# Performance work log

Hardware: AMD Instinct MI355X
Metric: run time of the kernel (lower is better)

The kernel has to match this reference:

```python
import jax, jax.numpy as jnp
import numpy as np

THRES = 0.5
EPS = 1e-8
FACTOR = 5


def _row_normalize(mx):
    # torch: rowsum over last dim, 1/rowsum with inf->0, diag @ mx == row scaling
    r_inv = 1.0 / mx.sum(-1)
    r_inv = jnp.where(jnp.isinf(r_inv), 0.0, r_inv)
    return mx * r_inv[..., None]


def _build_adj(feat):
    # cosine-similarity adjacency over rows of feat [B,N,D] -> [B,N,N]
    fn = feat / jnp.maximum(jnp.linalg.norm(feat, axis=-1, keepdims=True), EPS)
    sim = jnp.einsum('bnd,bmd->bnm', fn, fn)
    adj = (sim > THRES).astype(feat.dtype)
    adjT = jnp.swapaxes(adj, 1, 2)
    m = (adjT > adj).astype(feat.dtype)
    adj = adj + adjT * m - adj * m  # symmetric OR
    return _row_normalize(adj + jnp.eye(adj.shape[1], dtype=feat.dtype))


def _gcn(x, adj, w1, b1, w2, b2):
    # standard 2-layer pygcn: out = adj @ (x @ W) + b, relu between, dropout=0
    h = jax.nn.relu(jnp.einsum('bnm,bmf->bnf', adj, x @ w1) + b1)
    return jnp.einsum('bnm,bmf->bnf', adj, h @ w2) + b2


def setup_inputs() -> dict:
    key = jax.random.key(0)
    ks = jax.random.split(key, 13)
    B, C, HT = 1024, 64, 128   # batch, in_dim channels, height == feature_len
    FL, NH = 128, 8            # GCN nfeat/nclass, nhid
    s = lambda i, shape: jax.random.normal(ks[i], shape, jnp.float32) * 0.1
    return dict(
        x=jax.random.normal(ks[0], (B, C, HT), jnp.float32),
        wq=s(1, (C, C)), bq=s(2, (C,)),
        wk=s(3, (C, C)), bk=s(4, (C,)),
        wv=s(5, (C, C)), bv=s(6, (C,)),
        gw1=s(7, (FL, NH)), gb1=s(8, (NH,)),
        gw2=s(9, (NH, FL)), gb2=s(10, (FL,)),
        gamma=jax.random.normal(ks[11], (), jnp.float32),
        index_sample=jax.random.randint(ks[12], (HT, 25), 0, HT),  # (L_Q_inner, sample_k)
    )


def reference(x, wq, bq, wk, bk, wv, bv, gw1, gb1, gw2, gb2, gamma, index_sample):
    # 1x1 Conv1d projections: [B,C,H] -> [B,C,H]
    q = jnp.einsum('oc,bch->boh', wq, x) + bq[None, :, None]
    k = jnp.einsum('oc,bch->boh', wk, x) + bk[None, :, None]
    v = jnp.einsum('oc,bch->boh', wv, x) + bv[None, :, None]

    def branch(f):
        # source uses self.gcn_query for all three branches (faithful)
        return _gcn(_row_normalize(f), _build_adj(f), gw1, gb1, gw2, gb2)

    queries, keys, values = branch(q), branch(k), branch(v)
    B, L_Q, H = queries.shape        # [B, 64, 128]
    u = min(FACTOR * int(np.ceil(np.log(L_Q))), L_Q)  # n_top = 25

    # ProbSparse _prob_QK: inner view (B, Hn=64, Lk=128)
    Lk = keys.shape[2]
    Kg = keys[:, :, index_sample]                        # [B,64,Lk,S] gather
    qk_sample = jnp.einsum('bhl,bhls->bhs', queries, Kg)  # [B,64,S]
    M = qk_sample.max(-1) - qk_sample.sum(-1) / Lk        # [B,64]
    _, m_top = jax.lax.top_k(M, u)                        # [B,u] indices over node dim
    q_red = jnp.take_along_axis(queries, m_top[:, :, None], axis=1)  # [B,u,128]
    scores = jnp.einsum('bud,bnd->bun', q_red, keys) * (1.0 / np.sqrt(H))

    # mask_flag=True -> initial context is cumsum over nodes
    context = jnp.cumsum(values, axis=-2)                 # [B,64,128]
    attn = jax.nn.softmax(scores, axis=-1)
    upd = jnp.einsum('bun,bnd->bud', attn, values)        # [B,u,128]
    context = context.at[jnp.arange(B)[:, None], m_top].set(upd)
    return gamma * context + x
```

## Files before the change

kernel.cpp:

```cpp
#include <hip/hip_runtime.h>
#include <math.h>

#define T 1024
#define FS 132
#define FSQ 33
#define AS 68

typedef __attribute__((ext_vector_type(8)))  short short8;
typedef __attribute__((ext_vector_type(4)))  float f32x4;
typedef __attribute__((ext_vector_type(16))) float f32x16;
typedef __attribute__((ext_vector_type(4)))  unsigned u32x4;
typedef __attribute__((ext_vector_type(2)))  unsigned u32x2;

__device__ __forceinline__ void fma4(float4& a, float s, const float4 b) {
  a.x = fmaf(s, b.x, a.x);
  a.y = fmaf(s, b.y, a.y);
  a.z = fmaf(s, b.z, a.z);
  a.w = fmaf(s, b.w, a.w);
}
__device__ __forceinline__ unsigned bf16rne(float f) {
  unsigned u = __float_as_uint(f);
  return (u + 0x7FFFu + ((u >> 16) & 1u)) >> 16;
}
__device__ __forceinline__ void split3(float4 a, float4 b, short8& vh, short8& vm, short8& vl) {
  const float xs[8] = {a.x, a.y, a.z, a.w, b.x, b.y, b.z, b.w};
#pragma unroll
  for (int e = 0; e < 8; ++e) {
    float x = xs[e];
    unsigned h = bf16rne(x);
    float r1 = x - __uint_as_float(h << 16);
    unsigned m = bf16rne(r1);
    float r2 = r1 - __uint_as_float(m << 16);
    unsigned l2 = bf16rne(r2);
    vh[e] = (short)h; vm[e] = (short)m; vl[e] = (short)l2;
  }
}
__device__ __forceinline__ void split2(float4 a, float4 b, short8& vh, short8& vl) {
  const float xs[8] = {a.x, a.y, a.z, a.w, b.x, b.y, b.z, b.w};
#pragma unroll
  for (int e = 0; e < 8; ++e) {
    float x = xs[e];
    unsigned h = bf16rne(x);
    float r1 = x - __uint_as_float(h << 16);
    unsigned l2 = bf16rne(r1);
    vh[e] = (short)h; vl[e] = (short)l2;
  }
}
__device__ __forceinline__ f32x16 mm32(short8 a, short8 b, f32x16 c) {
  return __builtin_amdgcn_mfma_f32_32x32x16_bf16(a, b, c, 0, 0, 0);
}
__device__ __forceinline__ f32x4 mm16(short8 a, short8 b, f32x4 c) {
  return __builtin_amdgcn_mfma_f32_16x16x32_bf16(a, b, c, 0, 0, 0);
}

__global__ __launch_bounds__(T) void gcn_ssa_kernel(
    const float* __restrict__ x,
    const float* __restrict__ wq, const float* __restrict__ bq,
    const float* __restrict__ wk, const float* __restrict__ bk,
    const float* __restrict__ wv, const float* __restrict__ bv,
    const float* __restrict__ gw1, const float* __restrict__ gb1,
    const float* __restrict__ gw2, const float* __restrict__ gb2,
    const float* __restrict__ gammap, const int* __restrict__ idxg,
    float* __restrict__ out)
{
  const int b = blockIdx.x, tid = threadIdx.x;
  const int l = tid & 63;
  const int wid = tid >> 6;
  const float* xb = x + (size_t)b * 8192;
  float* outb = out + (size_t)b * 8192;

  __shared__ __align__(16) float fq[64 * FS];
  __shared__ __align__(16) float fk[64 * FS];
  __shared__ __align__(16) float fv[64 * FS];
  __shared__ __align__(16) float U[11904];
  __shared__ __align__(16) float gw1T[16 * FS];
  __shared__ __align__(16) float gb1s[8];
  __shared__ __align__(16) float gb2s[128];
  __shared__ float rinv_s[3][64], nrm_s[3][64], rinv2_s[3][64];
  __shared__ int mte[32];

  float4* fq4 = (float4*)fq;
  float4* fk4 = (float4*)fk;
  float4* fv4 = (float4*)fv;

  {
    const float4* xg = (const float4*)xb;
    for (int i = tid; i < 2048; i += T) {
      int c = i & 63, hq = i >> 6;
      float4 v = xg[c * 32 + hq];
      int h = hq * 4;
      U[(h + 0) * AS + c] = v.x;
      U[(h + 1) * AS + c] = v.y;
      U[(h + 2) * AS + c] = v.z;
      U[(h + 3) * AS + c] = v.w;
    }
    if (tid < 192) U[8704 + tid] = (tid < 64) ? bq[tid] : (tid < 128) ? bk[tid - 64] : bv[tid - 128];
    for (int i = tid; i < 2048; i += T) {
      int j = i >> 7, h = i & 127;
      gw1T[j * FS + h] = (j < 8) ? gw1[h * 8 + j] : 0.f;
    }
    if (tid < 8) gb1s[tid] = gb1[tid];
    if (tid < 128) gb2s[tid] = gb2[tid];
  }
  __syncthreads();

  if (wid < 12) {
    const int p = wid >> 2, strip = wid & 3;
    const float* wsel = (p == 0) ? wq : (p == 1) ? wk : wv;
    float* fdst = (p == 0) ? fq : (p == 1) ? fk : fv;
    const int lr = l & 31, kg = (l >> 5) * 4;
    const int h = strip * 32 + lr;
    f32x16 acc0 = (f32x16)0.f, acc1 = (f32x16)0.f;
    for (int ks = 0; ks < 4; ++ks) {
      int kb = ks * 16;
      float4 b0 = *(const float4*)(U + h * AS + kb + kg);
      float4 b1 = *(const float4*)(U + h * AS + kb + 8 + kg);
      short8 bh, bm, bl;
      split3(b0, b1, bh, bm, bl);
      float4 a0 = *(const float4*)(wsel + lr * 64 + kb + kg);
      float4 a1 = *(const float4*)(wsel + lr * 64 + kb + 8 + kg);
      short8 ah, am, al;
      split3(a0, a1, ah, am, al);
      acc0 = mm32(ah, bh, acc0); acc0 = mm32(ah, bm, acc0); acc0 = mm32(am, bh, acc0);
      acc0 = mm32(ah, bl, acc0); acc0 = mm32(al, bh, acc0); acc0 = mm32(am, bm, acc0);
      a0 = *(const float4*)(wsel + (32 + lr) * 64 + kb + kg);
      a1 = *(const float4*)(wsel + (32 + lr) * 64 + kb + 8 + kg);
      split3(a0, a1, ah, am, al);
      acc1 = mm32(ah, bh, acc1); acc1 = mm32(ah, bm, acc1); acc1 = mm32(am, bh, acc1);
      acc1 = mm32(ah, bl, acc1); acc1 = mm32(al, bh, acc1); acc1 = mm32(am, bm, acc1);
    }
#pragma unroll
    for (int reg = 0; reg < 16; ++reg) {
      int ro = (reg & 3) + 8 * (reg >> 2) + 4 * (l >> 5);
      fdst[ro * FS + h] = acc0[reg] + U[8704 + p * 64 + ro];
      fdst[(32 + ro) * FS + h] = acc1[reg] + U[8704 + p * 64 + 32 + ro];
    }
  }
  __syncthreads();

  {
    int row = tid >> 4, g = tid & 15;
#pragma unroll
    for (int br = 0; br < 3; ++br) {
      const float4* f4b = (br == 0) ? fq4 : (br == 1) ? fk4 : fv4;
      float4 aa = f4b[row * FSQ + 2 * g];
      float4 cc = f4b[row * FSQ + 2 * g + 1];
      float s0 = aa.x + aa.y + aa.z + aa.w + cc.x + cc.y + cc.z + cc.w;
      float s1 = aa.x * aa.x + aa.y * aa.y + aa.z * aa.z + aa.w * aa.w +
                 cc.x * cc.x + cc.y * cc.y + cc.z * cc.z + cc.w * cc.w;
      for (int off = 8; off; off >>= 1) {
        s0 += __shfl_xor(s0, off);
        s1 += __shfl_xor(s1, off);
      }
      if (g == 0) {
        rinv_s[br][row] = (s0 == 0.0f) ? 0.0f : (1.0f / s0);
        nrm_s[br][row] = 1.0f / fmaxf(sqrtf(s1), 1e-8f);
      }
    }
  }
  __syncthreads();

  unsigned short* adjw = (unsigned short*)U;
  float* t1T = U + 6912;
  float* hT  = U + 8544;
  float* gsm = U + 10176;

  if (wid < 12) {
    int br = wid >> 2, tile = wid & 3;
    const float* f = (br == 0) ? fq : (br == 1) ? fk : fv;
    int r0 = (tile >> 1) * 32, c0 = (tile & 1) * 32;
    int lr = l & 31, kg = (l >> 5) * 4;
    f32x16 acc = (f32x16)0.f;
    for (int ks = 0; ks < 8; ++ks) {
      int kb = ks * 16;
      float4 a0 = *(const float4*)(f + (r0 + lr) * FS + kb + kg);
      float4 a1 = *(const float4*)(f + (r0 + lr) * FS + kb + 8 + kg);
      float4 b0 = *(const float4*)(f + (c0 + lr) * FS + kb + kg);
      float4 b1 = *(const float4*)(f + (c0 + lr) * FS + kb + 8 + kg);
      short8 ah, am, al, bh, bm, bl;
      split3(a0, a1, ah, am, al);
      split3(b0, b1, bh, bm, bl);
      acc = mm32(ah, bh, acc); acc = mm32(ah, bm, acc); acc = mm32(am, bh, acc);
      acc = mm32(ah, bl, acc); acc = mm32(al, bh, acc); acc = mm32(am, bm, acc);
    }
    float nm = nrm_s[br][c0 + lr];
#pragma unroll
    for (int reg = 0; reg < 16; ++reg) {
      int rowg = r0 + (reg & 3) + 8 * (reg >> 2) + 4 * (l >> 5);
      int m = c0 + lr;
      float sim = acc[reg] * nrm_s[br][rowg] * nm;
      unsigned short e = (sim > 0.5f) ? (unsigned short)0x3F80 : (unsigned short)0;
      if (rowg == m) e = (sim > 0.5f) ? (unsigned short)0x4000 : (unsigned short)0x3F80;
      adjw[(br * 64 + rowg) * 72 + m] = e;
    }
  } else {
    int u = wid - 12;
    int j15 = l & 15, kg4 = (l >> 4) * 4;
    short8 gbh[4], gbm[4], gbl[4];
#pragma unroll
    for (int ks = 0; ks < 4; ++ks) {
      int kb = ks * 32;
      float4 b0 = *(const float4*)(gw1T + j15 * FS + kb + kg4);
      float4 b1 = *(const float4*)(gw1T + j15 * FS + kb + 16 + kg4);
      split3(b0, b1, gbh[ks], gbm[ks], gbl[ks]);
    }
#pragma unroll
    for (int i = 0; i < 3; ++i) {
      int tl = u * 3 + i;
      int br = tl >> 2, mt = tl & 3;
      const float* f = (br == 0) ? fq : (br == 1) ? fk : fv;
      f32x4 acc = (f32x4)0.f;
      for (int ks = 0; ks < 4; ++ks) {
        int kb = ks * 32;
        float4 a0 = *(const float4*)(f + (mt * 16 + j15) * FS + kb + kg4);
        float4 a1 = *(const float4*)(f + (mt * 16 + j15) * FS + kb + 16 + kg4);
        short8 ah, am, al;
        split3(a0, a1, ah, am, al);
        acc = mm16(ah, gbh[ks], acc); acc = mm16(ah, gbm[ks], acc); acc = mm16(am, gbh[ks], acc);
        acc = mm16(ah, gbl[ks], acc); acc = mm16(al, gbh[ks], acc); acc = mm16(am, gbm[ks], acc);
      }
      if (j15 < 8) {
#pragma unroll
        for (int r = 0; r < 4; ++r) {
          int n = mt * 16 + (l >> 4) * 4 + r;
          t1T[(br * 8 + j15) * AS + n] = acc[r] * rinv_s[br][n];
        }
      }
    }
  }
  __syncthreads();

  if (tid < 768) {
    int rid = tid >> 2, g = tid & 3;
    int br = rid >> 6, n = rid & 63;
    const unsigned short* rp = adjw + (br * 64 + n) * 72 + g * 16;
    u32x4 v0 = *(const u32x4*)rp;
    u32x4 v1 = *(const u32x4*)(rp + 8);
    unsigned wds[8] = {v0.x, v0.y, v0.z, v0.w, v1.x, v1.y, v1.z, v1.w};
    float s = 0.f;
#pragma unroll
    for (int e = 0; e < 8; ++e) {
      s += __uint_as_float(wds[e] << 16);
      s += __uint_as_float(wds[e] & 0xFFFF0000u);
    }
    s += __shfl_xor(s, 1);
    s += __shfl_xor(s, 2);
    if (g == 0) rinv2_s[br][n] = 1.0f / s;
  }
  __syncthreads();

  if (tid < 768) {
    int br = wid >> 2, mt = wid & 3;
    int j15 = l & 15, kg4 = (l >> 4) * 4;
    int arow = br * 64 + mt * 16 + j15;
    f32x4 acc = (f32x4)0.f;
#pragma unroll
    for (int ks = 0; ks < 2; ++ks) {
      int kb = ks * 32;
      u32x2 lo = *(const u32x2*)(adjw + arow * 72 + kb + kg4);
      u32x2 hi = *(const u32x2*)(adjw + arow * 72 + kb + 16 + kg4);
      u32x4 cc; cc.x = lo.x; cc.y = lo.y; cc.z = hi.x; cc.w = hi.y;
      short8 af = __builtin_bit_cast(short8, cc);
      float4 b0 = *(const float4*)(t1T + (br * 8 + j15) * AS + kb + kg4);
      float4 b1 = *(const float4*)(t1T + (br * 8 + j15) * AS + kb + 16 + kg4);
      short8 bh, bm, bl;
      split3(b0, b1, bh, bm, bl);
      acc = mm16(af, bh, acc); acc = mm16(af, bm, acc); acc = mm16(af, bl, acc);
    }
    if (j15 < 8) {
      float g1 = gb1s[j15];
#pragma unroll
      for (int r = 0; r < 4; ++r) {
        int n = mt * 16 + (l >> 4) * 4 + r;
        hT[(br * 8 + j15) * AS + n] = fmaxf(fmaf(acc[r], rinv2_s[br][n], g1), 0.0f);
      }
    }
  }
  __syncthreads();

  if (tid < 768) {
    int br = wid >> 2, mt = wid & 3;
    int j15 = l & 15, kg4 = (l >> 4) * 4;
    int arow = br * 64 + mt * 16 + j15;
    f32x4 acc = (f32x4)0.f;
#pragma unroll
    for (int ks = 0; ks < 2; ++ks) {
      int kb = ks * 32;
      u32x2 lo = *(const u32x2*)(adjw + arow * 72 + kb + kg4);
      u32x2 hi = *(const u32x2*)(adjw + arow * 72 + kb + 16 + kg4);
      u32x4 cc; cc.x = lo.x; cc.y = lo.y; cc.z = hi.x; cc.w = hi.y;
      short8 af = __builtin_bit_cast(short8, cc);
      float4 b0 = *(const float4*)(hT + (br * 8 + j15) * AS + kb + kg4);
      float4 b1 = *(const float4*)(hT + (br * 8 + j15) * AS + kb + 16 + kg4);
      short8 bh, bm, bl;
      split3(b0, b1, bh, bm, bl);
      acc = mm16(af, bh, acc); acc = mm16(af, bm, acc); acc = mm16(af, bl, acc);
    }
    if (j15 < 8) {
#pragma unroll
      for (int r = 0; r < 4; ++r) {
        int n = mt * 16 + (l >> 4) * 4 + r;
        gsm[(br * 64 + n) * 8 + j15] = acc[r] * rinv2_s[br][n];
      }
    }
  }
  __syncthreads();

  {
    int n0 = tid >> 5, hq = tid & 31;
    float4 wreg[8];
#pragma unroll
    for (int j = 0; j < 8; ++j) wreg[j] = ((const float4*)gw2)[j * 32 + hq];
    float4 bquad = ((const float4*)gb2s)[hq];
#pragma unroll
    for (int br = 0; br < 3; ++br) {
      float4* f4b = (br == 0) ? fq4 : (br == 1) ? fk4 : fv4;
#pragma unroll
      for (int half = 0; half < 2; ++half) {
        int n = n0 + 32 * half;
        const float* g = gsm + (br * 64 + n) * 8;
        float4 g0 = *(const float4*)g;
        float4 g1 = *(const float4*)(g + 4);
        float4 a = bquad;
        fma4(a, g0.x, wreg[0]); fma4(a, g0.y, wreg[1]); fma4(a, g0.z, wreg[2]); fma4(a, g0.w, wreg[3]);
        fma4(a, g1.x, wreg[4]); fma4(a, g1.y, wreg[5]); fma4(a, g1.z, wreg[6]); fma4(a, g1.w, wreg[7]);
        f4b[n * FSQ + hq] = a;
      }
    }
  }
  __syncthreads();

  float* kT = U;
  float* Pp = U + 8704;
  {
    const int c = tid >> 6;
    const int n = tid & 63;
    float4 v0 = fk4[n * FSQ + 2 * c];
    float4 v1 = fk4[n * FSQ + 2 * c + 1];
    const float* p0 = (const float*)&v0;
    const float* p1 = (const float*)&v1;
#pragma unroll
    for (int e = 0; e < 4; ++e) kT[(8 * c + e) * AS + n] = p0[e];
#pragma unroll
    for (int e = 0; e < 4; ++e) kT[(8 * c + 4 + e) * AS + n] = p1[e];
  }
  __syncthreads();

  const float gamma = *gammap;
  if (tid < 128) {
    const int w = tid >> 6, n = l;
    float acc[25];
#pragma unroll
    for (int s = 0; s < 25; ++s) acc[s] = 0.f;
    const float* qrow = fq + n * FS + w * 64;
    for (int lb = 0; lb < 16; ++lb) {
      float4 qv = *(const float4*)(qrow + 4 * lb);
      const float* qp = (const float*)&qv;
#pragma unroll
      for (int i = 0; i < 4; ++i) {
        const float qs = qp[i];
        const int base = __builtin_amdgcn_readfirstlane((w * 64 + 4 * lb + i) * 25);
#pragma unroll
        for (int s = 0; s < 25; ++s) {
          acc[s] = fmaf(qs, kT[idxg[base + s] * AS + n], acc[s]);
        }
      }
    }
    float* P = Pp + w * 1600;
#pragma unroll
    for (int s = 0; s < 25; ++s) P[s * 64 + n] = acc[s];
  } else if (tid < 256) {
    const int h = tid - 128;
    float acc = 0.f;
    for (int n = 0; n < 64; ++n) {
      acc += fv[n * FS + h];
      outb[n * 128 + h] = fmaf(gamma, acc, xb[n * 128 + h]);
    }
  }
  __syncthreads();

  if (tid < 64) {
    if (tid >= 25 && tid < 32) mte[tid] = 0;
    const float* P0 = Pp;
    const float* P1 = Pp + 1600;
    float mx = -INFINITY, su = 0.f;
#pragma unroll
    for (int s = 0; s < 25; ++s) {
      float vsum = P0[s * 64 + tid] + P1[s * 64 + tid];
      mx = fmaxf(mx, vsum);
      su += vsum;
    }
    float v = mx - su * (1.0f / 128.0f);
    for (int it = 0; it < 25; ++it) {
      float bv2 = v;
      int bi = tid;
#pragma unroll
      for (int off = 32; off > 0; off >>= 1) {
        float ov = __shfl_xor(bv2, off);
        int oi = __shfl_xor(bi, off);
        if (ov > bv2 || (ov == bv2 && oi < bi)) { bv2 = ov; bi = oi; }
      }
      if (tid == 0) mte[it] = bi;
      if (tid == bi) v = -INFINITY;
    }
  }
  __syncthreads();

  float* sc = U + 8704;
  float* vT = U;
  if (tid < 128) {
    const int wsc = tid >> 6;
    const int lr = l & 31;
    const int kg = (l >> 5) * 4;
    const int qr = mte[lr];
    const float scale = 0.08838834764831845f;
    f32x16 acc = (f32x16)0.f;
    for (int ks = 0; ks < 8; ++ks) {
      int kb = ks * 16;
      float4 a0 = *(const float4*)(fq + qr * FS + kb + kg);
      float4 a1 = *(const float4*)(fq + qr * FS + kb + 8 + kg);
      float4 b0 = *(const float4*)(fk + (wsc * 32 + lr) * FS + kb + kg);
      float4 b1 = *(const float4*)(fk + (wsc * 32 + lr) * FS + kb + 8 + kg);
      short8 ah, al2, bh, bl;
      split2(a0, a1, ah, al2);
      split2(b0, b1, bh, bl);
      acc = mm32(ah, bh, acc);
      acc = mm32(ah, bl, acc);
      acc = mm32(al2, bh, acc);
    }
#pragma unroll
    for (int reg = 0; reg < 16; ++reg) {
      int uu = (reg & 3) + 8 * (reg >> 2) + 4 * (l >> 5);
      if (uu < 25) sc[uu * AS + wsc * 32 + lr] = acc[reg] * scale;
    }
  } else {
    for (int i = tid - 128; i < 8192; i += 896) {
      int h2 = i >> 6, n = i & 63;
      vT[h2 * AS + n] = fv[n * FS + h2];
    }
  }
  __syncthreads();

  if (tid < 400) {
    int u = tid >> 4, g = tid & 15;
    float4* s4 = (float4*)(sc + u * AS);
    float4 v = s4[g];
    float mx = fmaxf(fmaxf(v.x, v.y), fmaxf(v.z, v.w));
    for (int off = 8; off; off >>= 1) mx = fmaxf(mx, __shfl_xor(mx, off));
    float4 e;
    e.x = __expf(v.x - mx); e.y = __expf(v.y - mx);
    e.z = __expf(v.z - mx); e.w = __expf(v.w - mx);
    float su = e.x + e.y + e.z + e.w;
    for (int off = 8; off; off >>= 1) su += __shfl_xor(su, off);
    float inv = 1.0f / su;
    e.x *= inv; e.y *= inv; e.z *= inv; e.w *= inv;
    s4[g] = e;
  }
  __syncthreads();

  if (tid < 512) {
    const int w8 = tid >> 6;
    const int li = l & 15;
    const int kg4 = (l >> 4) * 4;
#pragma unroll
    for (int i = 0; i < 2; ++i) {
      int t = w8 * 2 + i;
      int ut = t >> 3, ht = t & 7;
      int u = ut * 16 + li;
      f32x4 acc = (f32x4)0.f;
#pragma unroll
      for (int ks = 0; ks < 2; ++ks) {
        int kb = ks * 32;
        float4 a0 = *(const float4*)(sc + u * AS + kb + kg4);
        float4 a1 = *(const float4*)(sc + u * AS + kb + 16 + kg4);
        float4 b0 = *(const float4*)(vT + (ht * 16 + li) * AS + kb + kg4);
        float4 b1 = *(const float4*)(vT + (ht * 16 + li) * AS + kb + 16 + kg4);
        short8 ah, al2, bh, bl;
        split2(a0, a1, ah, al2);
        split2(b0, b1, bh, bl);
        acc = mm16(ah, bh, acc);
        acc = mm16(ah, bl, acc);
        acc = mm16(al2, bh, acc);
      }
      int hcol = ht * 16 + li;
#pragma unroll
      for (int r = 0; r < 4; ++r) {
        int uu = ut * 16 + (l >> 4) * 4 + r;
        if (uu < 25) {
          int row = mte[uu];
          int o = row * 128 + hcol;
          outb[o] = fmaf(gamma, acc[r], xb[o]);
        }
      }
    }
  }
}

extern "C" void kernel_launch(void* const* d_in, const int* in_sizes, int n_in,
                              void* d_out, int out_size, void* d_ws, size_t ws_size,
                              hipStream_t stream) {
  const float* x   = (const float*)d_in[0];
  const float* wq  = (const float*)d_in[1];
  const float* bq  = (const float*)d_in[2];
  const float* wk  = (const float*)d_in[3];
  const float* bk  = (const float*)d_in[4];
  const float* wv  = (const float*)d_in[5];
  const float* bv  = (const float*)d_in[6];
  const float* gw1 = (const float*)d_in[7];
  const float* gb1 = (const float*)d_in[8];
  const float* gw2 = (const float*)d_in[9];
  const float* gb2 = (const float*)d_in[10];
  const float* gm  = (const float*)d_in[11];
  const int* idx   = (const int*)d_in[12];
  float* out = (float*)d_out;
  int B = in_sizes[0] / (64 * 128);
  hipLaunchKernelGGL(gcn_ssa_kernel, dim3(B), dim3(T), 0, stream,
                     x, wq, bq, wk, bk, wv, bv, gw1, gb1, gw2, gb2, gm, idx, out);
}
```

Baseline: 296.6 us.

## Exploit adjacency symmetry, fuse rowsum into GCN stage, restage ProbSparse sampling

The similarity matmul now computes only the two diagonal 32x32 tiles and one off-diagonal tile per branch, mirroring the result into the transposed position, since the matrix is symmetric. That frees warps, which take on the X@W1 tiles. The adjacency row-sum is folded into the first GCN aggregation stage, removing one barrier. The sample indices are staged into LDS as packed ushorts, the Q-K sampling loop is reorganised so each lane handles two rows and half the samples, and the V transpose moves earlier to overlap with top-k selection. These changes cut redundant MFMA work, a synchronisation and repeated global index loads, at the cost of more complex indexing and possible LDS bank conflicts on the mirrored stores.

```diff
diff --git a/kernel.cpp b/kernel.cpp
--- a/kernel.cpp
+++ b/kernel.cpp
@@ -165,37 +165,58 @@
   float* hT  = U + 8544;
   float* gsm = U + 10176;
 
-  if (wid < 12) {
-    int br = wid >> 2, tile = wid & 3;
+  if (wid < 9) {
+    const int br = wid / 3, t3 = wid % 3;
     const float* f = (br == 0) ? fq : (br == 1) ? fk : fv;
-    int r0 = (tile >> 1) * 32, c0 = (tile & 1) * 32;
-    int lr = l & 31, kg = (l >> 5) * 4;
+    const int lr = l & 31, kg = (l >> 5) * 4;
     f32x16 acc = (f32x16)0.f;
-    for (int ks = 0; ks < 8; ++ks) {
-      int kb = ks * 16;
-      float4 a0 = *(const float4*)(f + (r0 + lr) * FS + kb + kg);
-      float4 a1 = *(const float4*)(f + (r0 + lr) * FS + kb + 8 + kg);
-      float4 b0 = *(const float4*)(f + (c0 + lr) * FS + kb + kg);
-      float4 b1 = *(const float4*)(f + (c0 + lr) * FS + kb + 8 + kg);
-      short8 ah, am, al, bh, bm, bl;
-      split3(a0, a1, ah, am, al);
-      split3(b0, b1, bh, bm, bl);
-      acc = mm32(ah, bh, acc); acc = mm32(ah, bm, acc); acc = mm32(am, bh, acc);
-      acc = mm32(ah, bl, acc); acc = mm32(al, bh, acc); acc = mm32(am, bm, acc);
-    }
-    float nm = nrm_s[br][c0 + lr];
-#pragma unroll
-    for (int reg = 0; reg < 16; ++reg) {
-      int rowg = r0 + (reg & 3) + 8 * (reg >> 2) + 4 * (l >> 5);
-      int m = c0 + lr;
-      float sim = acc[reg] * nrm_s[br][rowg] * nm;
-      unsigned short e = (sim > 0.5f) ? (unsigned short)0x3F80 : (unsigned short)0;
-      if (rowg == m) e = (sim > 0.5f) ? (unsigned short)0x4000 : (unsigned short)0x3F80;
-      adjw[(br * 64 + rowg) * 72 + m] = e;
+    if (t3 < 2) {
+      const int r0 = t3 * 32;
+      for (int ks = 0; ks < 8; ++ks) {
+        int kb = ks * 16;
+        float4 a0 = *(const float4*)(f + (r0 + lr) * FS + kb + kg);
+        float4 a1 = *(const float4*)(f + (r0 + lr) * FS + kb + 8 + kg);
+        short8 h, m, lo;
+        split3(a0, a1, h, m, lo);
+        acc = mm32(h, h, acc); acc = mm32(h, m, acc); acc = mm32(m, h, acc);
+        acc = mm32(h, lo, acc); acc = mm32(lo, h, acc); acc = mm32(m, m, acc);
+      }
+      float nm = nrm_s[br][r0 + lr];
+#pragma unroll
+      for (int reg = 0; reg < 16; ++reg) {
+        int rowg = r0 + (reg & 3) + 8 * (reg >> 2) + 4 * (l >> 5);
+        int m = r0 + lr;
+        float sim = acc[reg] * nrm_s[br][rowg] * nm;
+        unsigned short e = (sim > 0.5f) ? (unsigned short)0x3F80 : (unsigned short)0;
+        if (rowg == m) e = (sim > 0.5f) ? (unsigned short)0x4000 : (unsigned short)0x3F80;
+        adjw[(br * 64 + rowg) * 72 + m] = e;
+      }
+    } else {
+      for (int ks = 0; ks < 8; ++ks) {
+        int kb = ks * 16;
+        float4 a0 = *(const float4*)(f + lr * FS + kb + kg);
+        float4 a1 = *(const float4*)(f + lr * FS + kb + 8 + kg);
+        float4 b0 = *(const float4*)(f + (32 + lr) * FS + kb + kg);
+        float4 b1 = *(const float4*)(f + (32 + lr) * FS + kb + 8 + kg);
+        short8 ah, am, al, bh, bm, bl;
+        split3(a0, a1, ah, am, al);
+        split3(b0, b1, bh, bm, bl);
+        acc = mm32(ah, bh, acc); acc = mm32(ah, bm, acc); acc = mm32(am, bh, acc);
+        acc = mm32(ah, bl, acc); acc = mm32(al, bh, acc); acc = mm32(am, bm, acc);
+      }
+      float nm = nrm_s[br][32 + lr];
+#pragma unroll
+      for (int reg = 0; reg < 16; ++reg) {
+        int rowg = (reg & 3) + 8 * (reg >> 2) + 4 * (l >> 5);
+        int m = 32 + lr;
+        float sim = acc[reg] * nrm_s[br][rowg] * nm;
+        unsigned short e = (sim > 0.5f) ? (unsigned short)0x3F80 : (unsigned short)0;
+        adjw[(br * 64 + rowg) * 72 + m] = e;
+        adjw[(br * 64 + m) * 72 + rowg] = e;
+      }
     }
   } else {
-    int u = wid - 12;
-    int j15 = l & 15, kg4 = (l >> 4) * 4;
+    const int j15 = l & 15, kg4 = (l >> 4) * 4;
     short8 gbh[4], gbm[4], gbl[4];
 #pragma unroll
     for (int ks = 0; ks < 4; ++ks) {
@@ -205,54 +226,58 @@
       split3(b0, b1, gbh[ks], gbm[ks], gbl[ks]);
     }
 #pragma unroll
-    for (int i = 0; i < 3; ++i) {
-      int tl = u * 3 + i;
-      int br = tl >> 2, mt = tl & 3;
-      const float* f = (br == 0) ? fq : (br == 1) ? fk : fv;
-      f32x4 acc = (f32x4)0.f;
-      for (int ks = 0; ks < 4; ++ks) {
-        int kb = ks * 32;
-        float4 a0 = *(const float4*)(f + (mt * 16 + j15) * FS + kb + kg4);
-        float4 a1 = *(const float4*)(f + (mt * 16 + j15) * FS + kb + 16 + kg4);
-        short8 ah, am, al;
-        split3(a0, a1, ah, am, al);
-        acc = mm16(ah, gbh[ks], acc); acc = mm16(ah, gbm[ks], acc); acc = mm16(am, gbh[ks], acc);
-        acc = mm16(ah, gbl[ks], acc); acc = mm16(al, gbh[ks], acc); acc = mm16(am, gbm[ks], acc);
-      }
-      if (j15 < 8) {
-#pragma unroll
-        for (int r = 0; r < 4; ++r) {
-          int n = mt * 16 + (l >> 4) * 4 + r;
-          t1T[(br * 8 + j15) * AS + n] = acc[r] * rinv_s[br][n];
+    for (int rep = 0; rep < 2; ++rep) {
+      int t = (wid - 9) + rep * 7;
+      if (t < 12) {
+        int br = t >> 2, mt = t & 3;
+        const float* f = (br == 0) ? fq : (br == 1) ? fk : fv;
+        f32x4 acc = (f32x4)0.f;
+        for (int ks = 0; ks < 4; ++ks) {
+          int kb = ks * 32;
+          float4 a0 = *(const float4*)(f + (mt * 16 + j15) * FS + kb + kg4);
+          float4 a1 = *(const float4*)(f + (mt * 16 + j15) * FS + kb + 16 + kg4);
+          short8 ah, am, al;
+          split3(a0, a1, ah, am, al);
+          acc = mm16(ah, gbh[ks], acc); acc = mm16(ah, gbm[ks], acc); acc = mm16(am, gbh[ks], acc);
+          acc = mm16(ah, gbl[ks], acc); acc = mm16(al, gbh[ks], acc); acc = mm16(am, gbm[ks], acc);
         }
+        if (j15 < 8) {
+#pragma unroll
+          for (int r = 0; r < 4; ++r) {
+            int n = mt * 16 + (l >> 4) * 4 + r;
+            t1T[(br * 8 + j15) * AS + n] = acc[r] * rinv_s[br][n];
+          }
+        }
       }
     }
   }
   __syncthreads();
 
   if (tid < 768) {
-    int rid = tid >> 2, g = tid & 3;
-    int br = rid >> 6, n = rid & 63;
-    const unsigned short* rp = adjw + (br * 64 + n) * 72 + g * 16;
-    u32x4 v0 = *(const u32x4*)rp;
-    u32x4 v1 = *(const u32x4*)(rp + 8);
-    unsigned wds[8] = {v0.x, v0.y, v0.z, v0.w, v1.x, v1.y, v1.z, v1.w};
-    float s = 0.f;
-#pragma unroll
-    for (int e = 0; e < 8; ++e) {
-      s += __uint_as_float(wds[e] << 16);
-      s += __uint_as_float(wds[e] & 0xFFFF0000u);
-    }
-    s += __shfl_xor(s, 1);
-    s += __shfl_xor(s, 2);
-    if (g == 0) rinv2_s[br][n] = 1.0f / s;
-  }
-  __syncthreads();
-
-  if (tid < 768) {
-    int br = wid >> 2, mt = wid & 3;
-    int j15 = l & 15, kg4 = (l >> 4) * 4;
-    int arow = br * 64 + mt * 16 + j15;
+    const int br = wid >> 2, mt = wid & 3;
+    const int j15 = l & 15, kg4 = (l >> 4) * 4;
+    float rinv2;
+    {
+      const unsigned short* rp = adjw + (br * 64 + mt * 16 + j15) * 72 + (l >> 4) * 16;
+      u32x4 v0 = *(const u32x4*)rp;
+      u32x4 v1 = *(const u32x4*)(rp + 8);
+      unsigned wds[8] = {v0.x, v0.y, v0.z, v0.w, v1.x, v1.y, v1.z, v1.w};
+      float s = 0.f;
+#pragma unroll
+      for (int e = 0; e < 8; ++e) {
+        s += __uint_as_float(wds[e] << 16);
+        s += __uint_as_float(wds[e] & 0xFFFF0000u);
+      }
+      s += __shfl_xor(s, 16);
+      s += __shfl_xor(s, 32);
+      rinv2 = 1.0f / s;
+      if (l < 16) rinv2_s[br][mt * 16 + l] = rinv2;
+    }
+    float rv4[4];
+#pragma unroll
+    for (int r = 0; r < 4; ++r) rv4[r] = __shfl(rinv2, (l >> 4) * 4 + r);
+
+    const int arow = br * 64 + mt * 16 + j15;
     f32x4 acc = (f32x4)0.f;
 #pragma unroll
     for (int ks = 0; ks < 2; ++ks) {
@@ -272,16 +297,16 @@
 #pragma unroll
       for (int r = 0; r < 4; ++r) {
         int n = mt * 16 + (l >> 4) * 4 + r;
-        hT[(br * 8 + j15) * AS + n] = fmaxf(fmaf(acc[r], rinv2_s[br][n], g1), 0.0f);
+        hT[(br * 8 + j15) * AS + n] = fmaxf(fmaf(acc[r], rv4[r], g1), 0.0f);
       }
     }
   }
   __syncthreads();
 
   if (tid < 768) {
-    int br = wid >> 2, mt = wid & 3;
-    int j15 = l & 15, kg4 = (l >> 4) * 4;
-    int arow = br * 64 + mt * 16 + j15;
+    const int br = wid >> 2, mt = wid & 3;
+    const int j15 = l & 15, kg4 = (l >> 4) * 4;
+    const int arow = br * 64 + mt * 16 + j15;
     f32x4 acc = (f32x4)0.f;
 #pragma unroll
     for (int ks = 0; ks < 2; ++ks) {
@@ -332,6 +357,7 @@
 
   float* kT = U;
   float* Pp = U + 8704;
+  unsigned short* idxp = (unsigned short*)gw1T;
   {
     const int c = tid >> 6;
     const int n = tid & 63;
@@ -343,32 +369,60 @@
     for (int e = 0; e < 4; ++e) kT[(8 * c + e) * AS + n] = p0[e];
 #pragma unroll
     for (int e = 0; e < 4; ++e) kT[(8 * c + 4 + e) * AS + n] = p1[e];
+    for (int i = tid; i < 3200; i += T) {
+      int lr = i / 25, s = i - lr * 25;
+      idxp[lr * 32 + s] = (unsigned short)idxg[i];
+    }
   }
   __syncthreads();
 
   const float gamma = *gammap;
   if (tid < 128) {
-    const int w = tid >> 6, n = l;
-    float acc[25];
-#pragma unroll
-    for (int s = 0; s < 25; ++s) acc[s] = 0.f;
-    const float* qrow = fq + n * FS + w * 64;
+    const int w = wid;
+    const int na = l & 31;
+    const int sh = l >> 5;
+    const int s0 = sh ? 13 : 0;
+    const int scnt = sh ? 12 : 13;
+    float acc0[13], acc1[13];
+#pragma unroll
+    for (int si = 0; si < 13; ++si) { acc0[si] = 0.f; acc1[si] = 0.f; }
+    const float* q0 = fq + (2 * na) * FS + w * 64;
+    const float* q1 = q0 + FS;
     for (int lb = 0; lb < 16; ++lb) {
-      float4 qv = *(const float4*)(qrow + 4 * lb);
-      const float* qp = (const float*)&qv;
+      float4 qa = *(const float4*)(q0 + 4 * lb);
+      float4 qb = *(const float4*)(q1 + 4 * lb);
+      const float qs0[4] = {qa.x, qa.y, qa.z, qa.w};
+      const float qs1[4] = {qb.x, qb.y, qb.z, qb.w};
 #pragma unroll
       for (int i = 0; i < 4; ++i) {
-        const float qs = qp[i];
-        const int base = __builtin_amdgcn_readfirstlane((w * 64 + 4 * lb + i) * 25);
-#pragma unroll
-        for (int s = 0; s < 25; ++s) {
-          acc[s] = fmaf(qs, kT[idxg[base + s] * AS + n], acc[s]);
+        const int lrow = w * 64 + 4 * lb + i;
+        u32x4 i0 = *(const u32x4*)(idxp + lrow * 32);
+        u32x4 i1 = *(const u32x4*)(idxp + lrow * 32 + 8);
+        u32x4 i2 = *(const u32x4*)(idxp + lrow * 32 + 16);
+        unsigned i3 = *(const unsigned*)(idxp + lrow * 32 + 24);
+        unsigned iw[13] = {i0.x, i0.y, i0.z, i0.w, i1.x, i1.y, i1.z, i1.w,
+                           i2.x, i2.y, i2.z, i2.w, i3};
+        const float qv0 = qs0[i], qv1 = qs1[i];
+#pragma unroll
+        for (int si = 0; si < 13; ++si) {
+          if (si < scnt) {
+            int s = s0 + si;
+            unsigned ki = (iw[s >> 1] >> ((s & 1) * 16)) & 0xFFFFu;
+            float2 kv = *(const float2*)(kT + ki * AS + 2 * na);
+            acc0[si] = fmaf(qv0, kv.x, acc0[si]);
+            acc1[si] = fmaf(qv1, kv.y, acc1[si]);
+          }
         }
       }
     }
-    float* P = Pp + w * 1600;
-#pragma unroll
-    for (int s = 0; s < 25; ++s) P[s * 64 + n] = acc[s];
+#pragma unroll
+    for (int si = 0; si < 13; ++si) {
+      if (si < scnt) {
+        int s = s0 + si;
+        float2 pr; pr.x = acc0[si]; pr.y = acc1[si];
+        *(float2*)(Pp + (w * 25 + s) * 64 + 2 * na) = pr;
+      }
+    }
   } else if (tid < 256) {
     const int h = tid - 128;
     float acc = 0.f;
@@ -379,6 +433,7 @@
   }
   __syncthreads();
 
+  float* vT = U;
   if (tid < 64) {
     if (tid >= 25 && tid < 32) mte[tid] = 0;
     const float* P0 = Pp;
@@ -403,13 +458,17 @@
       if (tid == 0) mte[it] = bi;
       if (tid == bi) v = -INFINITY;
     }
+  } else if (tid >= 128) {
+    for (int i = tid - 128; i < 8192; i += 896) {
+      int h2 = i >> 6, n = i & 63;
+      vT[h2 * AS + n] = fv[n * FS + h2];
+    }
   }
   __syncthreads();
 
   float* sc = U + 8704;
-  float* vT = U;
   if (tid < 128) {
-    const int wsc = tid >> 6;
+    const int wsc = wid;
     const int lr = l & 31;
     const int kg = (l >> 5) * 4;
     const int qr = mte[lr];
@@ -433,11 +492,6 @@
       int uu = (reg & 3) + 8 * (reg >> 2) + 4 * (l >> 5);
       if (uu < 25) sc[uu * AS + wsc * 32 + lr] = acc[reg] * scale;
     }
-  } else {
-    for (int i = tid - 128; i < 8192; i += 896) {
-      int h2 = i >> 6, n = i & 63;
-      vT[h2 * AS + n] = fv[n * FS + h2];
-    }
   }
   __syncthreads();
 
@@ -459,7 +513,7 @@
   __syncthreads();
 
   if (tid < 512) {
-    const int w8 = tid >> 6;
+    const int w8 = wid;
     const int li = l & 15;
     const int kg4 = (l >> 4) * 4;
 #pragma unroll
```

Result: slower. 569.1 us (+91.9%).
